# Kernel optimization log

Hardware: AMD Instinct MI355X
Metric: run time of the kernel (lower is better)

## Reference

```python
import jax, jax.numpy as jnp
import numpy as np
import math

D_MODEL = 1024
NUM_HEADS = 16
D_K = D_MODEL // NUM_HEADS  # 64
THETA = 10000.0
B, S = 2, 2048


def setup_inputs() -> dict:
    key = jax.random.key(0)
    kx, kq, kk, kv, ko = jax.random.split(key, 5)
    sigma = (2.0 / (D_MODEL + D_MODEL)) ** 0.5
    return {
        "x": jax.random.normal(kx, (B, S, D_MODEL), dtype=jnp.float32),
        "Wq": jax.random.normal(kq, (D_MODEL, D_MODEL), dtype=jnp.float32) * sigma,
        "Wk": jax.random.normal(kk, (D_MODEL, D_MODEL), dtype=jnp.float32) * sigma,
        "Wv": jax.random.normal(kv, (D_MODEL, D_MODEL), dtype=jnp.float32) * sigma,
        "Wo": jax.random.normal(ko, (D_MODEL, D_MODEL), dtype=jnp.float32) * sigma,
        "token_positions": jnp.arange(S, dtype=jnp.int32),
    }


def _rope(x, token_positions):
    # x: [..., seq, d_k]; rotate interleaved even/odd pairs.
    half = x.shape[-1] // 2
    freq = jnp.power(THETA, -jnp.arange(0, x.shape[-1], 2, dtype=jnp.float32) / x.shape[-1])  # [half]
    angles = token_positions[:, None].astype(jnp.float32) * freq[None, :]  # [seq, half]
    cos, sin = jnp.cos(angles), jnp.sin(angles)
    x1 = x[..., 0::2]
    x2 = x[..., 1::2]
    out = jnp.stack([x1 * cos - x2 * sin, x1 * sin + x2 * cos], axis=-1)  # [..., seq, half, 2]
    return out.reshape(x.shape)


def reference(x, Wq, Wk, Wv, Wo, token_positions):
    Bb, Ss, Dm = x.shape
    H, Dk = NUM_HEADS, D_K
    # Linear: y = x @ W.T ; split as (n head) -> heads first
    def heads(y):
        return y.reshape(Bb, Ss, H, Dk).transpose(0, 2, 1, 3)  # [B,H,S,Dk]
    Q = heads(x @ Wq.T)
    K = heads(x @ Wk.T)
    V = heads(x @ Wv.T)
    Q = _rope(Q, token_positions)
    K = _rope(K, token_positions)
    scores = jnp.einsum("bhqd,bhkd->bhqk", Q, K) / math.sqrt(Dk)  # [B,H,S,S]
    causal = jnp.tril(jnp.ones((Ss, Ss), dtype=bool))
    scores = jnp.where(causal, scores, -jnp.inf)
    # original casts to fp64 for softmax; numerically-stable fp32 softmax here
    probs = jax.nn.softmax(scores, axis=-1)
    attn = jnp.einsum("bhqk,bhkd->bhqd", probs, V)  # [B,H,S,Dk]
    attn = attn.transpose(0, 2, 1, 3).reshape(Bb, Ss, Dm)
    return attn @ Wo.T
```

## Files before the change

kernel.cpp:

```cpp
#include <hip/hip_runtime.h>
#include <hip/hip_bf16.h>
#include <math.h>

typedef __bf16 bf16_t;
typedef __attribute__((ext_vector_type(8))) __bf16 bf16x8;
typedef __attribute__((ext_vector_type(4))) __bf16 bf16x4;
typedef __attribute__((ext_vector_type(4))) float f32x4;

#define B_DIM 2
#define S_DIM 2048
#define H_DIM 16
#define DK 64
#define DM 1024
#define KDIM 1024

#define MFMA(a, b, c) __builtin_amdgcn_mfma_f32_16x16x32_bf16((a), (b), (c), 0, 0, 0)

__device__ __forceinline__ void gload_lds16(const bf16_t* g, bf16_t* l) {
    __builtin_amdgcn_global_load_lds(
        (const __attribute__((address_space(1))) void*)g,
        (__attribute__((address_space(3))) void*)l, 16, 0, 0);
}

__global__ void cvt_kernel(const float* __restrict__ src, bf16_t* __restrict__ dst, int n) {
    int i = (blockIdx.x * blockDim.x + threadIdx.x) * 4;
    if (i >= n) return;
    float4 v = *reinterpret_cast<const float4*>(src + i);
    bf16x4 o;
    o[0] = (__bf16)v.x; o[1] = (__bf16)v.y; o[2] = (__bf16)v.z; o[3] = (__bf16)v.w;
    *reinterpret_cast<bf16x4*>(dst + i) = o;
}

__global__ void cvt4_kernel(const float* __restrict__ s0, const float* __restrict__ s1,
                            const float* __restrict__ s2, const float* __restrict__ s3,
                            bf16_t* __restrict__ d0, bf16_t* __restrict__ d1,
                            bf16_t* __restrict__ d2, bf16_t* __restrict__ d3, int n) {
    const float* s; bf16_t* d;
    switch (blockIdx.y) {
        case 0: s = s0; d = d0; break;
        case 1: s = s1; d = d1; break;
        case 2: s = s2; d = d2; break;
        default: s = s3; d = d3; break;
    }
    int i = (blockIdx.x * blockDim.x + threadIdx.x) * 4;
    if (i >= n) return;
    float4 v = *reinterpret_cast<const float4*>(s + i);
    bf16x4 o;
    o[0] = (__bf16)v.x; o[1] = (__bf16)v.y; o[2] = (__bf16)v.z; o[3] = (__bf16)v.w;
    *reinterpret_cast<bf16x4*>(d + i) = o;
}

template <int MODE>
__global__ __launch_bounds__(256)
void gemm_bt(const bf16_t* __restrict__ A,
             const bf16_t* __restrict__ B0,
             const bf16_t* __restrict__ B1,
             const bf16_t* __restrict__ B2,
             bf16_t* __restrict__ outQ,
             bf16_t* __restrict__ outK,
             bf16_t* __restrict__ outVt,
             float* __restrict__ outF,
             const int* __restrict__ pos) {
    constexpr int CP = 136;
    __shared__ bf16_t smem[(MODE == 0) ? (128 * CP) : 8192];
    bf16_t* As = smem;
    bf16_t* Bs = smem + 4096;
    bf16_t* Cs = smem;

    const int t = threadIdx.x;
    const int z = blockIdx.z;
    const bf16_t* Bm = (MODE == 0) ? (z == 0 ? B0 : (z == 1 ? B1 : B2)) : B0;

    const int m0 = blockIdx.x * 128;
    const int n0 = blockIdx.y * 128;
    const int lane = t & 63;
    const int w = t >> 6;
    const int wr = w >> 1;
    const int wc = w & 1;

    f32x4 acc[4][4] = {};

    const int ar = t >> 2;
    const int ac = (t & 3) * 8;
    const bf16_t* Ag = A + (size_t)m0 * KDIM;
    const bf16_t* Bg = Bm + (size_t)n0 * KDIM;

    const int rr = lane & 15;
    const int ko = (lane >> 4) * 8;

    for (int k0 = 0; k0 < KDIM; k0 += 32) {
        gload_lds16(Ag + (size_t)ar * KDIM + k0 + ac,        &As[t * 8]);
        gload_lds16(Ag + (size_t)(ar + 64) * KDIM + k0 + ac, &As[2048 + t * 8]);
        gload_lds16(Bg + (size_t)ar * KDIM + k0 + ac,        &Bs[t * 8]);
        gload_lds16(Bg + (size_t)(ar + 64) * KDIM + k0 + ac, &Bs[2048 + t * 8]);
        __syncthreads();

        bf16x8 af[4], bfr[4];
#pragma unroll
        for (int m = 0; m < 4; ++m)
            af[m] = *reinterpret_cast<const bf16x8*>(&As[(wr * 64 + m * 16 + rr) * 32 + ko]);
#pragma unroll
        for (int n = 0; n < 4; ++n)
            bfr[n] = *reinterpret_cast<const bf16x8*>(&Bs[(wc * 64 + n * 16 + rr) * 32 + ko]);
#pragma unroll
        for (int m = 0; m < 4; ++m)
#pragma unroll
            for (int n = 0; n < 4; ++n)
                acc[m][n] = MFMA(af[m], bfr[n], acc[m][n]);
        __syncthreads();
    }

    const int rlb = wr * 64 + (lane >> 4) * 4;
    const int clb = wc * 64 + (lane & 15);

    if (MODE == 0) {
        if (z < 2) {
#pragma unroll
            for (int m = 0; m < 4; ++m)
#pragma unroll
                for (int n = 0; n < 4; ++n)
#pragma unroll
                    for (int j = 0; j < 4; ++j)
                        Cs[(rlb + m * 16 + j) * CP + clb + n * 16] = (__bf16)acc[m][n][j];
            __syncthreads();

            bf16_t* dst = (z == 0) ? outQ : outK;
            const int dch = t & 7;
            const int srow = t >> 3;
            float fr[4];
#pragma unroll
            for (int i = 0; i < 4; ++i)
                fr[i] = exp2f((float)(dch * 4 + i) * -0.4152410118609203f);
#pragma unroll
            for (int p = 0; p < 4; ++p) {
                const int s_loc = p * 32 + srow;
                const int gm = m0 + s_loc;
                const int bb = gm >> 11, sg = gm & (S_DIM - 1);
                const float pv = (float)pos[sg];
                float csv[4], snv[4];
#pragma unroll
                for (int i = 0; i < 4; ++i) {
                    const float a = pv * fr[i];
                    csv[i] = cosf(a); snv[i] = sinf(a);
                }
#pragma unroll
                for (int hc = 0; hc < 2; ++hc) {
                    const bf16x8 vv = *reinterpret_cast<const bf16x8*>(
                        &Cs[s_loc * CP + hc * 64 + dch * 8]);
                    bf16x8 ov;
#pragma unroll
                    for (int i = 0; i < 4; ++i) {
                        const float v0 = (float)vv[2 * i], v1 = (float)vv[2 * i + 1];
                        ov[2 * i]     = (__bf16)(v0 * csv[i] - v1 * snv[i]);
                        ov[2 * i + 1] = (__bf16)(v0 * snv[i] + v1 * csv[i]);
                    }
                    const int h = (n0 >> 6) + hc;
                    *reinterpret_cast<bf16x8*>(
                        &dst[((size_t)(bb * H_DIM + h) * S_DIM + sg) * 64 + dch * 8]) = ov;
                }
            }
        } else {
#pragma unroll
            for (int m = 0; m < 4; ++m)
#pragma unroll
                for (int n = 0; n < 4; ++n) {
                    const int cl = clb + n * 16;
                    bf16x4 v4;
#pragma unroll
                    for (int j = 0; j < 4; ++j) v4[j] = (__bf16)acc[m][n][j];
                    *reinterpret_cast<bf16x4*>(&Cs[cl * CP + rlb + m * 16]) = v4;
                }
            __syncthreads();

            const int cl = t >> 1, sh = t & 1;
            const int cg = n0 + cl, h = cg >> 6, d = cg & 63;
            const int bb = m0 >> 11, s0g = m0 & (S_DIM - 1);
            bf16_t* vdst = &outVt[((size_t)(bb * H_DIM + h) * DK + d) * S_DIM + s0g + sh * 64];
#pragma unroll
            for (int i = 0; i < 8; ++i)
                *reinterpret_cast<bf16x8*>(&vdst[i * 8]) =
                    *reinterpret_cast<const bf16x8*>(&Cs[cl * CP + sh * 64 + i * 8]);
        }
    } else {
        const int rbase = m0 + rlb;
        const int cbase = n0 + clb;
#pragma unroll
        for (int m = 0; m < 4; ++m)
#pragma unroll
            for (int n = 0; n < 4; ++n)
#pragma unroll
                for (int j = 0; j < 4; ++j)
                    outF[(size_t)(rbase + m * 16 + j) * DM + cbase + n * 16] = acc[m][n][j];
    }
}

__global__ __launch_bounds__(256)
void attn_kernel(const bf16_t* __restrict__ Q, const bf16_t* __restrict__ Kg,
                 const bf16_t* __restrict__ Vt, bf16_t* __restrict__ O) {
    constexpr int PSTR = 72;
    __shared__ bf16_t Ks[2][64 * 64];
    __shared__ bf16_t Vs[2][64 * 64];
    __shared__ bf16_t P_lds[4][2][16 * PSTR];

    const int t = threadIdx.x;
    const int lane = t & 63;
    const int w = t >> 6;
    const int bh = blockIdx.x >> 4;
    const int qi = blockIdx.x & 15;
    const int qbH = 31 - qi, qbL = qi;
    const int q0H = qbH * 64 + w * 16;
    const int q0L = qbL * 64 + w * 16;
    const int b = bh >> 4, h = bh & 15;
    const int rr = lane & 15;
    const int hi = lane >> 4;

    const bf16_t* Kbh = Kg + (size_t)bh * S_DIM * DK;
    const bf16_t* Vbh = Vt + (size_t)bh * DK * S_DIM;
    bf16_t* PwH = P_lds[w][0];
    bf16_t* PwL = P_lds[w][1];

    const int i0 = t, i1 = t + 256;
    const int r0 = i0 >> 3, c0 = ((i0 & 7) ^ (r0 & 7)) * 8;
    const int r1 = i1 >> 3, c1 = ((i1 & 7) ^ (r1 & 7)) * 8;

    const float QSCALE = 0.18033688011112042f;
    const bf16_t* QpH = Q + ((size_t)bh * S_DIM + q0H) * DK;
    const bf16_t* QpL = Q + ((size_t)bh * S_DIM + q0L) * DK;
    bf16x8 qfH[2], qfL[2];
    qfH[0] = *reinterpret_cast<const bf16x8*>(&QpH[rr * DK + hi * 8]);
    qfH[1] = *reinterpret_cast<const bf16x8*>(&QpH[rr * DK + 32 + hi * 8]);
    qfL[0] = *reinterpret_cast<const bf16x8*>(&QpL[rr * DK + hi * 8]);
    qfL[1] = *reinterpret_cast<const bf16x8*>(&QpL[rr * DK + 32 + hi * 8]);
#pragma unroll
    for (int i = 0; i < 8; ++i) {
        qfH[0][i] = (__bf16)((float)qfH[0][i] * QSCALE);
        qfH[1][i] = (__bf16)((float)qfH[1][i] * QSCALE);
        qfL[0][i] = (__bf16)((float)qfL[0][i] * QSCALE);
        qfL[1][i] = (__bf16)((float)qfL[1][i] * QSCALE);
    }

    bf16x8 ones;
#pragma unroll
    for (int i = 0; i < 8; ++i) ones[i] = (__bf16)1.0f;

    f32x4 oH[4] = {}, oL[4] = {};
    f32x4 laH = {}, laL = {};
    float mH = -INFINITY, mL = -INFINITY;

    const int ntH = qbH + 1;

    gload_lds16(Kbh + (size_t)r0 * DK + c0, &Ks[0][i0 * 8]);
    gload_lds16(Kbh + (size_t)r1 * DK + c1, &Ks[0][i1 * 8]);
    gload_lds16(Vbh + (size_t)r0 * S_DIM + c0, &Vs[0][i0 * 8]);
    gload_lds16(Vbh + (size_t)r1 * S_DIM + c1, &Vs[0][i1 * 8]);
    __syncthreads();

    for (int tt = 0; tt < ntH; ++tt) {
        const int cur = tt & 1;
        const int kv0 = tt * 64;
        const bool doL = (tt <= qbL);

        if (tt + 1 < ntH) {
            const int kv1 = kv0 + 64;
            bf16_t* Kn = Ks[cur ^ 1];
            bf16_t* Vn = Vs[cur ^ 1];
            gload_lds16(Kbh + (size_t)(kv1 + r0) * DK + c0, &Kn[i0 * 8]);
            gload_lds16(Kbh + (size_t)(kv1 + r1) * DK + c1, &Kn[i1 * 8]);
            gload_lds16(Vbh + (size_t)r0 * S_DIM + kv1 + c0, &Vn[i0 * 8]);
            gload_lds16(Vbh + (size_t)r1 * S_DIM + kv1 + c1, &Vn[i1 * 8]);
        }
        const bf16_t* Kc = Ks[cur];
        const bf16_t* Vc = Vs[cur];

        f32x4 sH[4] = {}, sL[4] = {};
        __builtin_amdgcn_s_setprio(1);
#pragma unroll
        for (int t16 = 0; t16 < 4; ++t16) {
            const int r = t16 * 16 + rr;
            const int sw = (r & 7) * 8;
            bf16x8 kf0 = *reinterpret_cast<const bf16x8*>(&Kc[r * 64 + ((hi * 8) ^ sw)]);
            bf16x8 kf1 = *reinterpret_cast<const bf16x8*>(&Kc[r * 64 + ((32 + hi * 8) ^ sw)]);
            sH[t16] = MFMA(kf0, qfH[0], sH[t16]);
            sH[t16] = MFMA(kf1, qfH[1], sH[t16]);
            if (doL) {
                sL[t16] = MFMA(kf0, qfL[0], sL[t16]);
                sL[t16] = MFMA(kf1, qfL[1], sL[t16]);
            }
        }
        __builtin_amdgcn_s_setprio(0);

        if (tt == qbH) {
            const int qg = q0H + rr;
#pragma unroll
            for (int t16 = 0; t16 < 4; ++t16)
#pragma unroll
                for (int j = 0; j < 4; ++j)
                    if (kv0 + t16 * 16 + hi * 4 + j > qg) sH[t16][j] = -INFINITY;
        }
        if (tt == qbL) {
            const int qg = q0L + rr;
#pragma unroll
            for (int t16 = 0; t16 < 4; ++t16)
#pragma unroll
                for (int j = 0; j < 4; ++j)
                    if (kv0 + t16 * 16 + hi * 4 + j > qg) sL[t16][j] = -INFINITY;
        }

        {
            f32x4 mv = sH[0];
#pragma unroll
            for (int t16 = 1; t16 < 4; ++t16) {
                mv[0] = fmaxf(mv[0], sH[t16][0]); mv[1] = fmaxf(mv[1], sH[t16][1]);
                mv[2] = fmaxf(mv[2], sH[t16][2]); mv[3] = fmaxf(mv[3], sH[t16][3]);
            }
            const float mloc = fmaxf(fmaxf(mv[0], mv[1]), fmaxf(mv[2], mv[3]));
            if (__any(mloc - mH > 8.0f)) {
                float mf = fmaxf(mloc, __shfl_xor(mloc, 16));
                mf = fmaxf(mf, __shfl_xor(mf, 32));
                const float mnew = fmaxf(mH, mf);
                const float scale = exp2f(mH - mnew);
#pragma unroll
                for (int i = 0; i < 4; ++i) laH[i] *= scale;
#pragma unroll
                for (int db = 0; db < 4; ++db)
#pragma unroll
                    for (int j = 0; j < 4; ++j) oH[db][j] *= scale;
                mH = mnew;
            }
#pragma unroll
            for (int t16 = 0; t16 < 4; ++t16) {
                bf16x4 pb;
#pragma unroll
                for (int j = 0; j < 4; ++j) pb[j] = (__bf16)exp2f(sH[t16][j] - mH);
                *reinterpret_cast<bf16x4*>(&PwH[rr * PSTR + t16 * 16 + hi * 4]) = pb;
            }
        }
        if (doL) {
            f32x4 mv = sL[0];
#pragma unroll
            for (int t16 = 1; t16 < 4; ++t16) {
                mv[0] = fmaxf(mv[0], sL[t16][0]); mv[1] = fmaxf(mv[1], sL[t16][1]);
                mv[2] = fmaxf(mv[2], sL[t16][2]); mv[3] = fmaxf(mv[3], sL[t16][3]);
            }
            const float mloc = fmaxf(fmaxf(mv[0], mv[1]), fmaxf(mv[2], mv[3]));
            if (__any(mloc - mL > 8.0f)) {
                float mf = fmaxf(mloc, __shfl_xor(mloc, 16));
                mf = fmaxf(mf, __shfl_xor(mf, 32));
                const float mnew = fmaxf(mL, mf);
                const float scale = exp2f(mL - mnew);
#pragma unroll
                for (int i = 0; i < 4; ++i) laL[i] *= scale;
#pragma unroll
                for (int db = 0; db < 4; ++db)
#pragma unroll
                    for (int j = 0; j < 4; ++j) oL[db][j] *= scale;
                mL = mnew;
            }
#pragma unroll
            for (int t16 = 0; t16 < 4; ++t16) {
                bf16x4 pb;
#pragma unroll
                for (int j = 0; j < 4; ++j) pb[j] = (__bf16)exp2f(sL[t16][j] - mL);
                *reinterpret_cast<bf16x4*>(&PwL[rr * PSTR + t16 * 16 + hi * 4]) = pb;
            }
        }

        bf16x8 pH0 = *reinterpret_cast<const bf16x8*>(&PwH[rr * PSTR + hi * 8]);
        bf16x8 pH1 = *reinterpret_cast<const bf16x8*>(&PwH[rr * PSTR + 32 + hi * 8]);
        bf16x8 pL0, pL1;
        if (doL) {
            pL0 = *reinterpret_cast<const bf16x8*>(&PwL[rr * PSTR + hi * 8]);
            pL1 = *reinterpret_cast<const bf16x8*>(&PwL[rr * PSTR + 32 + hi * 8]);
        }
        __builtin_amdgcn_s_setprio(1);
        laH = MFMA(ones, pH0, laH);
        laH = MFMA(ones, pH1, laH);
        if (doL) {
            laL = MFMA(ones, pL0, laL);
            laL = MFMA(ones, pL1, laL);
        }
#pragma unroll
        for (int db = 0; db < 4; ++db) {
            const int vr = db * 16 + rr;
            const int sw = (vr & 7) * 8;
            bf16x8 vf0 = *reinterpret_cast<const bf16x8*>(&Vc[vr * 64 + ((hi * 8) ^ sw)]);
            bf16x8 vf1 = *reinterpret_cast<const bf16x8*>(&Vc[vr * 64 + ((32 + hi * 8) ^ sw)]);
            oH[db] = MFMA(vf0, pH0, oH[db]);
            oH[db] = MFMA(vf1, pH1, oH[db]);
            if (doL) {
                oL[db] = MFMA(vf0, pL0, oL[db]);
                oL[db] = MFMA(vf1, pL1, oL[db]);
            }
        }
        __builtin_amdgcn_s_setprio(0);

        __syncthreads();
    }

    {
        const float linv = 1.0f / laH[0];
#pragma unroll
        for (int db = 0; db < 4; ++db) {
            bf16x4 ov;
#pragma unroll
            for (int j = 0; j < 4; ++j) ov[j] = (__bf16)(oH[db][j] * linv);
            *reinterpret_cast<bf16x4*>(
                &O[((size_t)(b * S_DIM + q0H + rr)) * DM + h * DK + db * 16 + hi * 4]) = ov;
        }
    }
    {
        const float linv = 1.0f / laL[0];
#pragma unroll
        for (int db = 0; db < 4; ++db) {
            bf16x4 ov;
#pragma unroll
            for (int j = 0; j < 4; ++j) ov[j] = (__bf16)(oL[db][j] * linv);
            *reinterpret_cast<bf16x4*>(
                &O[((size_t)(b * S_DIM + q0L + rr)) * DM + h * DK + db * 16 + hi * 4]) = ov;
        }
    }
}

extern "C" void kernel_launch(void* const* d_in, const int* in_sizes, int n_in,
                              void* d_out, int out_size, void* d_ws, size_t ws_size,
                              hipStream_t stream) {
    const float* x  = (const float*)d_in[0];
    const float* Wq = (const float*)d_in[1];
    const float* Wk = (const float*)d_in[2];
    const float* Wv = (const float*)d_in[3];
    const float* Wo = (const float*)d_in[4];
    const int* pos  = (const int*)d_in[5];
    float* out = (float*)d_out;

    char* ws = (char*)d_ws;
    bf16_t* xb  = (bf16_t*)(ws);
    bf16_t* Wqb = (bf16_t*)(ws + (8u << 20));
    bf16_t* Wkb = (bf16_t*)(ws + (10u << 20));
    bf16_t* Wvb = (bf16_t*)(ws + (12u << 20));
    bf16_t* Wob = (bf16_t*)(ws + (14u << 20));
    bf16_t* Qb  = (bf16_t*)(ws + (16u << 20));
    bf16_t* Kb  = (bf16_t*)(ws + (24u << 20));
    bf16_t* Vtb = (bf16_t*)(ws + (32u << 20));
    bf16_t* Ab  = (bf16_t*)(ws);

    const int NX = B_DIM * S_DIM * DM;
    const int NW = DM * DM;

    cvt_kernel<<<NX / 1024, 256, 0, stream>>>(x, xb, NX);
    cvt4_kernel<<<dim3(NW / 1024, 4), 256, 0, stream>>>(Wq, Wk, Wv, Wo,
                                                        Wqb, Wkb, Wvb, Wob, NW);

    gemm_bt<0><<<dim3(32, 8, 3), 256, 0, stream>>>(xb, Wqb, Wkb, Wvb,
                                                   Qb, Kb, Vtb, nullptr, pos);

    attn_kernel<<<B_DIM * H_DIM * 16, 256, 0, stream>>>(Qb, Kb, Vtb, Ab);

    gemm_bt<1><<<dim3(32, 8, 1), 256, 0, stream>>>(Ab, Wob, nullptr, nullptr,
                                                   nullptr, nullptr, nullptr, out, pos);
}
```

Measured before the change: 136.2 us.

## Double GEMM K-tile to 64 with XOR-swizzled LDS and merge conversion kernels

Each main-loop step of the bf16 GEMM now loads a 64-wide K slice instead of 32, which halves the number of barrier pairs per tile. The LDS layout gets an XOR swizzle on 16-byte chunks to avoid bank conflicts on the MFMA fragment reads, and the MFMA block is wrapped in s_setprio. The two fp32-to-bf16 conversion kernels are merged into one launch covering x and all four weights. In exchange, the GEMM doubles its LDS use for staging and the fragment arrays raise register pressure.

```diff
diff --git a/kernel.cpp b/kernel.cpp
--- a/kernel.cpp
+++ b/kernel.cpp
@@ -22,32 +22,31 @@
         (__attribute__((address_space(3))) void*)l, 16, 0, 0);
 }
 
-__global__ void cvt_kernel(const float* __restrict__ src, bf16_t* __restrict__ dst, int n) {
-    int i = (blockIdx.x * blockDim.x + threadIdx.x) * 4;
-    if (i >= n) return;
-    float4 v = *reinterpret_cast<const float4*>(src + i);
+__global__ void cvt_all(const float* __restrict__ x,
+                        const float* __restrict__ wq, const float* __restrict__ wk,
+                        const float* __restrict__ wv, const float* __restrict__ wo,
+                        bf16_t* __restrict__ xb,
+                        bf16_t* __restrict__ wqb, bf16_t* __restrict__ wkb,
+                        bf16_t* __restrict__ wvb, bf16_t* __restrict__ wob) {
+    const long NX = (long)B_DIM * S_DIM * DM;
+    const long i = ((long)blockIdx.x * 256 + threadIdx.x) * 4;
+    const float* s; bf16_t* d; long off;
+    if (i < NX) { s = x; d = xb; off = i; }
+    else {
+        const long j = i - NX;
+        const int wsel = (int)(j >> 20);
+        off = j & ((1L << 20) - 1);
+        switch (wsel) {
+            case 0: s = wq; d = wqb; break;
+            case 1: s = wk; d = wkb; break;
+            case 2: s = wv; d = wvb; break;
+            default: s = wo; d = wob; break;
+        }
+    }
+    float4 v = *reinterpret_cast<const float4*>(s + off);
     bf16x4 o;
     o[0] = (__bf16)v.x; o[1] = (__bf16)v.y; o[2] = (__bf16)v.z; o[3] = (__bf16)v.w;
-    *reinterpret_cast<bf16x4*>(dst + i) = o;
-}
-
-__global__ void cvt4_kernel(const float* __restrict__ s0, const float* __restrict__ s1,
-                            const float* __restrict__ s2, const float* __restrict__ s3,
-                            bf16_t* __restrict__ d0, bf16_t* __restrict__ d1,
-                            bf16_t* __restrict__ d2, bf16_t* __restrict__ d3, int n) {
-    const float* s; bf16_t* d;
-    switch (blockIdx.y) {
-        case 0: s = s0; d = d0; break;
-        case 1: s = s1; d = d1; break;
-        case 2: s = s2; d = d2; break;
-        default: s = s3; d = d3; break;
-    }
-    int i = (blockIdx.x * blockDim.x + threadIdx.x) * 4;
-    if (i >= n) return;
-    float4 v = *reinterpret_cast<const float4*>(s + i);
-    bf16x4 o;
-    o[0] = (__bf16)v.x; o[1] = (__bf16)v.y; o[2] = (__bf16)v.z; o[3] = (__bf16)v.w;
-    *reinterpret_cast<bf16x4*>(d + i) = o;
+    *reinterpret_cast<bf16x4*>(d + off) = o;
 }
 
 template <int MODE>
@@ -62,9 +61,10 @@
              float* __restrict__ outF,
              const int* __restrict__ pos) {
     constexpr int CP = 136;
-    __shared__ bf16_t smem[(MODE == 0) ? (128 * CP) : 8192];
+    constexpr int SELEMS = (MODE == 0) ? (128 * CP) : 16384;
+    __shared__ bf16_t smem[SELEMS];
     bf16_t* As = smem;
-    bf16_t* Bs = smem + 4096;
+    bf16_t* Bs = smem + 8192;
     bf16_t* Cs = smem;
 
     const int t = threadIdx.x;
@@ -80,33 +80,58 @@
 
     f32x4 acc[4][4] = {};
 
-    const int ar = t >> 2;
-    const int ac = (t & 3) * 8;
     const bf16_t* Ag = A + (size_t)m0 * KDIM;
     const bf16_t* Bg = Bm + (size_t)n0 * KDIM;
 
     const int rr = lane & 15;
     const int ko = (lane >> 4) * 8;
 
-    for (int k0 = 0; k0 < KDIM; k0 += 32) {
-        gload_lds16(Ag + (size_t)ar * KDIM + k0 + ac,        &As[t * 8]);
-        gload_lds16(Ag + (size_t)(ar + 64) * KDIM + k0 + ac, &As[2048 + t * 8]);
-        gload_lds16(Bg + (size_t)ar * KDIM + k0 + ac,        &Bs[t * 8]);
-        gload_lds16(Bg + (size_t)(ar + 64) * KDIM + k0 + ac, &Bs[2048 + t * 8]);
+    int rI[4], cI[4];
+#pragma unroll
+    for (int c = 0; c < 4; ++c) {
+        const int i = t + c * 256;
+        rI[c] = i >> 3;
+        cI[c] = ((i & 7) ^ (rI[c] & 7)) * 8;
+    }
+
+    for (int k0 = 0; k0 < KDIM; k0 += 64) {
+#pragma unroll
+        for (int c = 0; c < 4; ++c) {
+            const int i = t + c * 256;
+            gload_lds16(Ag + (size_t)rI[c] * KDIM + k0 + cI[c], &As[i * 8]);
+        }
+#pragma unroll
+        for (int c = 0; c < 4; ++c) {
+            const int i = t + c * 256;
+            gload_lds16(Bg + (size_t)rI[c] * KDIM + k0 + cI[c], &Bs[i * 8]);
+        }
         __syncthreads();
 
-        bf16x8 af[4], bfr[4];
-#pragma unroll
-        for (int m = 0; m < 4; ++m)
-            af[m] = *reinterpret_cast<const bf16x8*>(&As[(wr * 64 + m * 16 + rr) * 32 + ko]);
-#pragma unroll
-        for (int n = 0; n < 4; ++n)
-            bfr[n] = *reinterpret_cast<const bf16x8*>(&Bs[(wc * 64 + n * 16 + rr) * 32 + ko]);
-#pragma unroll
-        for (int m = 0; m < 4; ++m)
-#pragma unroll
-            for (int n = 0; n < 4; ++n)
-                acc[m][n] = MFMA(af[m], bfr[n], acc[m][n]);
+        bf16x8 af[2][4], bfr[2][4];
+#pragma unroll
+        for (int kk = 0; kk < 2; ++kk) {
+#pragma unroll
+            for (int m = 0; m < 4; ++m) {
+                const int r = wr * 64 + m * 16 + rr;
+                af[kk][m] = *reinterpret_cast<const bf16x8*>(
+                    &As[r * 64 + ((kk * 32 + ko) ^ ((r & 7) * 8))]);
+            }
+#pragma unroll
+            for (int n = 0; n < 4; ++n) {
+                const int r = wc * 64 + n * 16 + rr;
+                bfr[kk][n] = *reinterpret_cast<const bf16x8*>(
+                    &Bs[r * 64 + ((kk * 32 + ko) ^ ((r & 7) * 8))]);
+            }
+        }
+        __builtin_amdgcn_s_setprio(1);
+#pragma unroll
+        for (int kk = 0; kk < 2; ++kk)
+#pragma unroll
+            for (int m = 0; m < 4; ++m)
+#pragma unroll
+                for (int n = 0; n < 4; ++n)
+                    acc[m][n] = MFMA(af[kk][m], bfr[kk][n], acc[m][n]);
+        __builtin_amdgcn_s_setprio(0);
         __syncthreads();
     }
 
@@ -445,10 +470,10 @@
 
     const int NX = B_DIM * S_DIM * DM;
     const int NW = DM * DM;
-
-    cvt_kernel<<<NX / 1024, 256, 0, stream>>>(x, xb, NX);
-    cvt4_kernel<<<dim3(NW / 1024, 4), 256, 0, stream>>>(Wq, Wk, Wv, Wo,
-                                                        Wqb, Wkb, Wvb, Wob, NW);
+    const int NTOT = NX + 4 * NW;
+
+    cvt_all<<<NTOT / 1024, 256, 0, stream>>>(x, Wq, Wk, Wv, Wo,
+                                             xb, Wqb, Wkb, Wvb, Wob);
 
     gemm_bt<0><<<dim3(32, 8, 3), 256, 0, stream>>>(xb, Wqb, Wkb, Wvb,
                                                    Qb, Kb, Vtb, nullptr, pos);
```

Measured after the change: 129.8 us. 1.05x faster.
